# Kernel tuning notes

Measured on AMD Instinct MI355X. Metric: run time of the kernel, lower is better.

The kernel has to match this reference:

```python
import jax, jax.numpy as jnp
import numpy as np

EMBED = 768
HEADS = 12
HEAD = EMBED // HEADS  # 64
NO_ROPE = 1
GRID = 32
S_IMG = GRID * GRID
SEQ = S_IMG + NO_ROPE
BATCH = 8
SCALE = HEAD ** -0.5


def _rope_tables():
    # VisionRotaryEmbeddingFast(dim=half_head_dim=HEAD//2, pt_seq_len=GRID)
    dim = HEAD // 2  # 32 per spatial axis
    inv_freq = 1.0 / (10000.0 ** (np.arange(0, dim, 2, dtype=np.float32) / dim))  # [dim//2]
    t = np.arange(GRID, dtype=np.float32)
    f = t[:, None] * inv_freq[None, :]              # [GRID, dim//2]
    f = np.repeat(f, 2, axis=-1)                    # interleaved pairs -> [GRID, dim]
    fh = np.broadcast_to(f[:, None, :], (GRID, GRID, dim))
    fw = np.broadcast_to(f[None, :, :], (GRID, GRID, dim))
    freqs = np.concatenate([fh, fw], axis=-1).reshape(S_IMG, HEAD)  # [S_IMG, HEAD]
    return jnp.asarray(np.cos(freqs)), jnp.asarray(np.sin(freqs))

ROPE_COS, ROPE_SIN = _rope_tables()


def _rel_pos_index():
    ch, cw = np.meshgrid(np.arange(GRID), np.arange(GRID), indexing='ij')
    coords = np.stack([ch.ravel(), cw.ravel()])          # [2, S_IMG]
    rel = coords[:, :, None] - coords[:, None, :]        # [2, S_IMG, S_IMG]
    rel = rel.transpose(1, 2, 0).astype(np.int64)
    rel[:, :, 0] += GRID - 1
    rel[:, :, 1] += GRID - 1
    rel[:, :, 0] *= 2 * GRID - 1
    return jnp.asarray(rel.sum(-1))                      # [S_IMG, S_IMG]

REL_INDEX = _rel_pos_index()


def _rotate_half(x):
    # pairs are interleaved: (d r) with r=2
    x2 = x.reshape(*x.shape[:-1], -1, 2)
    return jnp.stack([-x2[..., 1], x2[..., 0]], axis=-1).reshape(x.shape)


def _apply_rope(t):
    # t: [B, H, S, HEAD]; first NO_ROPE tokens bypass rope
    t_cls, t_img = t[:, :, :NO_ROPE, :], t[:, :, NO_ROPE:, :]
    t_img = t_img * ROPE_COS + _rotate_half(t_img) * ROPE_SIN
    return jnp.concatenate([t_cls, t_img], axis=2)


def setup_inputs() -> dict:
    key = jax.random.key(0)
    ks = jax.random.split(key, 6)
    std = EMBED ** -0.5
    return {
        'x': jax.random.normal(ks[0], (BATCH, SEQ, EMBED), jnp.float32),
        'qkv_w': jax.random.normal(ks[1], (3 * EMBED, EMBED), jnp.float32) * std,
        'qkv_b': jnp.zeros((3 * EMBED,), jnp.float32),
        'proj_w': jax.random.normal(ks[2], (EMBED, EMBED), jnp.float32) * std,
        'proj_b': jnp.zeros((EMBED,), jnp.float32),
        'rel_bias_table': jax.random.normal(ks[3], ((2 * GRID - 1) * (2 * GRID - 1), HEADS), jnp.float32) * 0.02,
        'key_padding_mask': jnp.zeros((BATCH, SEQ), jnp.bool_),
    }


def reference(x, qkv_w, qkv_b, proj_w, proj_b, rel_bias_table, key_padding_mask):
    B, S, _ = x.shape
    qkv = x @ qkv_w.T + qkv_b                                  # [B,S,3E]
    qkv = qkv.reshape(B, S, 3, HEADS, HEAD).transpose(2, 0, 3, 1, 4)
    q, k, v = qkv[0], qkv[1], qkv[2]                            # [B,H,S,D]
    q = _apply_rope(q)
    k = _apply_rope(k)
    scores = jnp.einsum('bhqd,bhkd->bhqk', q, k) * SCALE        # [B,H,S,S]
    # relative position bias on image-token sub-block
    bias = rel_bias_table[REL_INDEX]                            # [S_IMG,S_IMG,H]
    bias = bias.transpose(2, 0, 1)                              # [H,S_IMG,S_IMG]
    scores = scores.at[:, :, NO_ROPE:, NO_ROPE:].add(bias[None])
    neg = jnp.finfo(scores.dtype).min
    scores = jnp.where(key_padding_mask[:, None, None, :], neg, scores)
    attn = jax.nn.softmax(scores, axis=-1)
    ctx = jnp.einsum('bhqk,bhkd->bhqd', attn, v)
    ctx = ctx.transpose(0, 2, 1, 3).reshape(B, S, EMBED)
    return ctx @ proj_w.T + proj_b
```

## Files before the change

kernel.cpp:

```cpp
#include <hip/hip_runtime.h>
#include <math.h>

#define EMBED 768
#define NHEADS 12
#define HDIM 64
#define SEQ 1025
#define NBATCH 8
#define BHCOUNT (NBATCH*NHEADS)
#define MROWS (NBATCH*SEQ)
#define QKV_N (3*EMBED)
#define QKV_ELEMS (BHCOUNT*SEQ*HDIM)
#define BT_N 3969
#define MASKPAD 1088
#define QMUL 0.1803368801111204f
#define LOG2E 1.4426950408889634f
#define NX4 1574400
#define NW4 442368
#define NP4 147456

typedef __attribute__((ext_vector_type(8))) short bf16x8;
typedef __attribute__((ext_vector_type(4))) float f32x4;
typedef __attribute__((ext_vector_type(16))) float f32x16;
typedef __attribute__((ext_vector_type(4))) unsigned int u32x4;

static __device__ inline unsigned short f2bf(float f) {
    unsigned u = __float_as_uint(f);
    unsigned r = (u + 0x7FFF + ((u >> 16) & 1)) >> 16;
    return (unsigned short)r;
}

static __device__ inline unsigned int cvtpk(float a, float b) {
    unsigned int r;
    asm("v_cvt_pk_bf16_f32 %0, %1, %2" : "=v"(r) : "v"(a), "v"(b));
    return r;
}

static __device__ inline void gld16(const unsigned short* g, unsigned short* l) {
    __builtin_amdgcn_global_load_lds(
        (const __attribute__((address_space(1))) unsigned int*)g,
        (__attribute__((address_space(3))) unsigned int*)l,
        16, 0, 0);
}

__global__ __launch_bounds__(256)
void f2bf3_kernel(const float* __restrict__ x, const float* __restrict__ w,
                  const float* __restrict__ pw,
                  unsigned short* __restrict__ xbf, unsigned short* __restrict__ wbf,
                  unsigned short* __restrict__ pwbf)
{
    int i = blockIdx.x * 256 + threadIdx.x;
    const float* src; unsigned short* dst; int off;
    if (i < NX4)            { src = x;  dst = xbf;  off = i; }
    else if (i < NX4 + NW4) { src = w;  dst = wbf;  off = i - NX4; }
    else if (i < NX4 + NW4 + NP4) { src = pw; dst = pwbf; off = i - NX4 - NW4; }
    else return;
    float4 v = *reinterpret_cast<const float4*>(&src[off << 2]);
    ushort4 o;
    o.x = f2bf(v.x); o.y = f2bf(v.y); o.z = f2bf(v.z); o.w = f2bf(v.w);
    *reinterpret_cast<ushort4*>(&dst[off << 2]) = o;
}

__global__ __launch_bounds__(256)
void setup_tables_kernel(const float* __restrict__ bt, float* __restrict__ btT,
                         const unsigned char* __restrict__ m, unsigned char* __restrict__ mp,
                         float* __restrict__ cosT, float* __restrict__ sinT)
{
    const int bid = blockIdx.x, tid = threadIdx.x;
    if (bid < 256) {
        int s = (bid << 2) + (tid >> 6);
        int d = tid & 63;
        int pos = (d < 32) ? (s >> 5) : (s & 31);
        int j = (d & 31) >> 1;
        float ang = (float)pos * expf(-(float)j * 0.5756462732485115f);
        cosT[(s << 6) + d] = cosf(ang);
        sinT[(s << 6) + d] = sinf(ang);
    } else if (bid < 256 + 187) {
        int e = (bid - 256) * 256 + tid;
        if (e < NHEADS * BT_N) {
            int h = e / BT_N, idx = e - h * BT_N;
            btT[h * BT_N + idx] = bt[idx * NHEADS + h] * LOG2E;
        }
    } else {
        int b = bid - 443;
        for (int i = tid; i < MASKPAD; i += 256)
            mp[b * MASKPAD + i] = (i < SEQ) ? m[b * SEQ + i] : (unsigned char)0;
    }
}

__global__ __launch_bounds__(256)
void qkv_mfma_kernel(const unsigned short* __restrict__ xbf,
                     const unsigned short* __restrict__ wbf,
                     const float* __restrict__ bias,
                     const float* __restrict__ cosT, const float* __restrict__ sinT,
                     unsigned short* __restrict__ qout, unsigned short* __restrict__ kout,
                     unsigned short* __restrict__ vout)
{
    __shared__ unsigned short As[128][32];
    __shared__ unsigned short Bs[128][32];
    const int m0 = blockIdx.x * 128;
    const int n0 = blockIdx.y * 128;
    const int tid = threadIdx.x;
    const int w = tid >> 6, lane = tid & 63;
    const int li = lane & 15, lg = lane >> 4;
    const int wr = w >> 1, wc = w & 1;

    f32x4 acc[4][4];
    #pragma unroll
    for (int mi = 0; mi < 4; ++mi)
        #pragma unroll
        for (int nj = 0; nj < 4; ++nj) acc[mi][nj] = (f32x4){0.f, 0.f, 0.f, 0.f};

    for (int kt = 0; kt < 24; ++kt) {
        const int k0 = kt << 5;
        #pragma unroll
        for (int c = 0; c < 2; ++c) {
            const int idx = c * 256 + tid;
            const int row = idx >> 2, slot = idx & 3;
            int grow = m0 + row; if (grow > MROWS - 1) grow = MROWS - 1;
            gld16(&xbf[(long)grow * EMBED + k0 + slot * 8], &As[0][0] + idx * 8);
            gld16(&wbf[(long)(n0 + row) * EMBED + k0 + slot * 8], &Bs[0][0] + idx * 8);
        }
        __syncthreads();

        bf16x8 af[4], bfr[4];
        #pragma unroll
        for (int mi = 0; mi < 4; ++mi)
            af[mi] = *reinterpret_cast<const bf16x8*>(&As[wr * 64 + mi * 16 + li][lg * 8]);
        #pragma unroll
        for (int nj = 0; nj < 4; ++nj)
            bfr[nj] = *reinterpret_cast<const bf16x8*>(&Bs[wc * 64 + nj * 16 + li][lg * 8]);
        __builtin_amdgcn_s_setprio(1);
        #pragma unroll
        for (int mi = 0; mi < 4; ++mi)
            #pragma unroll
            for (int nj = 0; nj < 4; ++nj)
                acc[mi][nj] = __builtin_amdgcn_mfma_f32_16x16x32_bf16(
                    af[mi], bfr[nj], acc[mi][nj], 0, 0, 0);
        __builtin_amdgcn_s_setprio(0);
        __syncthreads();
    }

    int brow[4][4], srow[4][4];
    #pragma unroll
    for (int mi = 0; mi < 4; ++mi)
        #pragma unroll
        for (int r = 0; r < 4; ++r) {
            int m = m0 + wr * 64 + mi * 16 + lg * 4 + r;
            int mm = (m < MROWS) ? m : (MROWS - 1);
            int bb = mm / SEQ;
            brow[mi][r] = bb;
            srow[mi][r] = mm - bb * SEQ;
        }

    #pragma unroll
    for (int nj = 0; nj < 4; ++nj) {
        const int n = n0 + wc * 64 + nj * 16 + li;
        const int which = n / EMBED;
        const int nh = n - which * EMBED;
        const int h = nh >> 6, d = nh & 63;
        unsigned short* outp = (which == 0) ? qout : (which == 1) ? kout : vout;
        const float mul = (which == 0) ? QMUL : 1.0f;
        const float bn = bias[n];
        const bool dorope = which < 2;
        const float sgn = (d & 1) ? 1.f : -1.f;
        #pragma unroll
        for (int mi = 0; mi < 4; ++mi)
            #pragma unroll
            for (int r = 0; r < 4; ++r) {
                const int m = m0 + wr * 64 + mi * 16 + lg * 4 + r;
                float v = acc[mi][nj][r] + bn;
                float pv = __shfl_xor(v, 1, 64);
                if (m < MROWS) {
                    const int bb = brow[mi][r], s = srow[mi][r];
                    if (dorope && s >= 1) {
                        const int p = s - 1;
                        v = v * cosT[(p << 6) + d] + sgn * pv * sinT[(p << 6) + d];
                    }
                    outp[((long)(bb * NHEADS + h) * SEQ + s) * HDIM + d] = f2bf(v * mul);
                }
            }
    }
}

__global__ __launch_bounds__(256)
void attn_mfma_kernel(const unsigned short* __restrict__ qg,
                      const unsigned short* __restrict__ kg,
                      const unsigned short* __restrict__ vg,
                      const float* __restrict__ btT,
                      const unsigned char* __restrict__ maskpad,
                      unsigned short* __restrict__ ctx)
{
    __shared__ unsigned short Ks[2][64][64];
    __shared__ unsigned short Vts[2][64][64];

    const int i = (int)blockIdx.x;
    const int xcd = i & 7, jb = i >> 3;
    const int bh = xcd * 12 + (jb % 12);
    const int q0 = (jb / 12) * 128;
    const int b = bh / NHEADS, h = bh % NHEADS;
    const int tid = threadIdx.x;
    const int w = tid >> 6;
    const int lane = tid & 63;
    const int l31 = lane & 31;
    const int hi = lane >> 5;

    const unsigned short* qbase = qg + (long)bh * (SEQ * HDIM);
    const unsigned short* kbase = kg + (long)bh * (SEQ * HDIM);
    const unsigned short* vbase = vg + (long)bh * (SEQ * HDIM);
    const unsigned char* maskp = maskpad + b * MASKPAD;
    const float* btTh = btT + h * BT_N;

    const int sidx0 = tid, sidx1 = 256 + tid;
    const int sr0 = sidx0 >> 3, sc0 = (sidx0 & 7) << 3;
    const int sr1 = sidx1 >> 3, sc1 = (sidx1 & 7) << 3;
    const int kswz0 = ((sr0 ^ (sr0 >> 3)) & 7) << 3;
    const int kswz1 = ((sr1 ^ (sr1 >> 3)) & 7) << 3;

    gld16(&kbase[(long)sr0 * HDIM + (sc0 ^ kswz0)], &Ks[0][0][0] + sidx0 * 8);
    gld16(&kbase[(long)sr1 * HDIM + (sc1 ^ kswz1)], &Ks[0][0][0] + sidx1 * 8);
    int4 vreg[2];
    vreg[0] = *reinterpret_cast<const int4*>(&vbase[(long)sr0 * HDIM + sc0]);
    vreg[1] = *reinterpret_cast<const int4*>(&vbase[(long)sr1 * HDIM + sc1]);

    const int qrow = (w << 5) + l31;
    const int qi_l = q0 + qrow;
    const int qiq = (qi_l > SEQ - 1) ? (SEQ - 1) : qi_l;
    bf16x8 qf[4];
    #pragma unroll
    for (int s = 0; s < 4; ++s)
        qf[s] = *reinterpret_cast<const bf16x8*>(&qbase[(long)qiq * HDIM + s * 16 + hi * 8]);

    const float bq = (qi_l >= 1) ? 1.0f : 0.0f;
    int qp = qi_l - 1; if (qp < 0) qp = 0; if (qp > 1023) qp = 1023;
    const int qcode = (qp >> 5) * 63 + (qp & 31) + 1984;

    __syncthreads();
    {
        union { int4 v; unsigned short u[8]; } t0, t1;
        t0.v = vreg[0]; t1.v = vreg[1];
        const int cb30 = sc0 >> 3, cb31 = sc1 >> 3;
        #pragma unroll
        for (int e = 0; e < 8; ++e) {
            Vts[0][sc0 + e][sr0 ^ (((e ^ cb30) & 7) << 3)] = t0.u[e];
            Vts[0][sc1 + e][sr1 ^ (((e ^ cb31) & 7) << 3)] = t1.u[e];
        }
    }
    __syncthreads();

    float m_l = -1e30f, l_l = 0.f;
    f32x16 acco[2];
    #pragma unroll
    for (int r = 0; r < 16; ++r) { acco[0][r] = 0.f; acco[1][r] = 0.f; }

    int kcb[2][4];
    for (int kt = 0; kt < 17; ++kt) {
        const int k0 = kt * 64;
        const int cur = kt & 1;

        if (kt < 16) {
            const int k0n = k0 + 64;
            vreg[0] = (k0n + sr0 < SEQ)
                ? *reinterpret_cast<const int4*>(&vbase[(long)(k0n + sr0) * HDIM + sc0])
                : make_int4(0, 0, 0, 0);
            vreg[1] = (k0n + sr1 < SEQ)
                ? *reinterpret_cast<const int4*>(&vbase[(long)(k0n + sr1) * HDIM + sc1])
                : make_int4(0, 0, 0, 0);
            int ki0 = k0n + sr0; if (ki0 > SEQ - 1) ki0 = SEQ - 1;
            int ki1 = k0n + sr1; if (ki1 > SEQ - 1) ki1 = SEQ - 1;
            gld16(&kbase[(long)ki0 * HDIM + (sc0 ^ kswz0)], &Ks[cur ^ 1][0][0] + sidx0 * 8);
            gld16(&kbase[(long)ki1 * HDIM + (sc1 ^ kswz1)], &Ks[cur ^ 1][0][0] + sidx1 * 8);
        }

        unsigned int b4[2][4];
        float bvf[2][16];
        if (kt >= 1 && kt <= 15) {
            #pragma unroll
            for (int j = 0; j < 2; ++j)
                #pragma unroll
                for (int t = 0; t < 4; ++t) {
                    b4[j][t] = *reinterpret_cast<const unsigned int*>(
                        &maskp[k0 + j * 32 + t * 8 + hi * 4]);
                    kcb[j][t] += 126;
                    const int base = qcode - kcb[j][t];
                    if (t == 0 && hi == 0) {
                        float4 f = *reinterpret_cast<const float4*>(&btTh[base - 34]);
                        bvf[j][0] = btTh[base]; bvf[j][1] = f.z;
                        bvf[j][2] = f.y;        bvf[j][3] = f.x;
                    } else {
                        float4 f = *reinterpret_cast<const float4*>(&btTh[base - 3]);
                        bvf[j][t * 4 + 0] = f.w; bvf[j][t * 4 + 1] = f.z;
                        bvf[j][t * 4 + 2] = f.y; bvf[j][t * 4 + 3] = f.x;
                    }
                }
        } else {
            #pragma unroll
            for (int j = 0; j < 2; ++j)
                #pragma unroll
                for (int t = 0; t < 4; ++t) {
                    unsigned int bb = 0;
                    #pragma unroll
                    for (int ri = 0; ri < 4; ++ri) {
                        const int ki = k0 + j * 32 + t * 8 + hi * 4 + ri;
                        const int kic = (ki > SEQ - 1) ? (SEQ - 1) : ki;
                        unsigned int dead = (ki >= SEQ) ? 1u : (unsigned int)maskp[kic];
                        bb |= (dead ? 1u : 0u) << (ri * 8);
                        int kp = ki - 1; if (kp < 0) kp = 0; if (kp > 1023) kp = 1023;
                        const int kcv = (kp >> 5) * 63 + (kp & 31);
                        bvf[j][t * 4 + ri] = btTh[qcode - kcv];
                    }
                    b4[j][t] = bb;
                    if (kt == 0) {
                        const int kp0 = j * 32 + t * 8 + hi * 4 - 1;
                        kcb[j][t] = (kp0 >> 5) * 63 + (kp0 & 31);
                    }
                }
        }

        f32x16 accs[2];
        #pragma unroll
        for (int r = 0; r < 16; ++r) { accs[0][r] = 0.f; accs[1][r] = 0.f; }
        __builtin_amdgcn_s_setprio(1);
        #pragma unroll
        for (int j = 0; j < 2; ++j) {
            const int rswz = ((l31 ^ (j * 4 + (l31 >> 3))) & 7) << 3;
            const unsigned short* krow = &Ks[cur][j * 32 + l31][0];
            #pragma unroll
            for (int s = 0; s < 4; ++s) {
                bf16x8 kf = *reinterpret_cast<const bf16x8*>(&krow[(s * 16 + hi * 8) ^ rswz]);
                accs[j] = __builtin_amdgcn_mfma_f32_32x32x16_bf16(kf, qf[s], accs[j], 0, 0, 0);
            }
        }
        __builtin_amdgcn_s_setprio(0);

        const float bq00 = (kt == 0 && hi == 0) ? 0.0f : bq;
        accs[0][0] += bvf[0][0] * bq00;
        #pragma unroll
        for (int j = 0; j < 2; ++j)
            #pragma unroll
            for (int r = 0; r < 16; ++r)
                if (!(j == 0 && r == 0))
                    accs[j][r] += bvf[j][r] * bq;
        if (__any((b4[0][0] | b4[0][1] | b4[0][2] | b4[0][3] |
                   b4[1][0] | b4[1][1] | b4[1][2] | b4[1][3]) != 0)) {
            #pragma unroll
            for (int j = 0; j < 2; ++j)
                #pragma unroll
                for (int r = 0; r < 16; ++r)
                    if ((b4[j][r >> 2] >> ((r & 3) * 8)) & 0xFF) accs[j][r] = -1e30f;
        }

        float mx = accs[0][0];
        #pragma unroll
        for (int j = 0; j < 2; ++j)
            #pragma unroll
            for (int r = 0; r < 16; ++r) mx = fmaxf(mx, accs[j][r]);
        mx = fmaxf(mx, __shfl_xor(mx, 32, 64));
        if (__any(mx > m_l + 8.0f)) {
            const float mnew = fmaxf(m_l, mx);
            const float alpha = __builtin_amdgcn_exp2f(m_l - mnew);
            #pragma unroll
            for (int r = 0; r < 16; ++r) {
                const float al = __shfl(alpha, (r & 3) + 8 * (r >> 2) + 4 * hi, 64);
                acco[0][r] *= al;
                acco[1][r] *= al;
            }
            l_l *= alpha;
            m_l = mnew;
        }
        float rs = 0.f;
        #pragma unroll
        for (int j = 0; j < 2; ++j)
            #pragma unroll
            for (int r = 0; r < 16; ++r) {
                accs[j][r] = __builtin_amdgcn_exp2f(accs[j][r] - m_l);
                rs += accs[j][r];
            }
        rs += __shfl_xor(rs, 32, 64);
        l_l += rs;

        unsigned int W[2][8];
        #pragma unroll
        for (int j = 0; j < 2; ++j)
            #pragma unroll
            for (int p = 0; p < 8; ++p)
                W[j][p] = cvtpk(accs[j][2 * p], accs[j][2 * p + 1]);
        #pragma unroll
        for (int j = 0; j < 2; ++j)
            #pragma unroll
            for (int sg = 0; sg < 2; ++sg) {
                unsigned int a0 = W[j][4 * sg + 0], a2 = W[j][4 * sg + 2];
                asm volatile("v_permlane32_swap_b32 %0, %1" : "+v"(a0), "+v"(a2));
                W[j][4 * sg + 0] = a0; W[j][4 * sg + 2] = a2;
                unsigned int a1 = W[j][4 * sg + 1], a3 = W[j][4 * sg + 3];
                asm volatile("v_permlane32_swap_b32 %0, %1" : "+v"(a1), "+v"(a3));
                W[j][4 * sg + 1] = a1; W[j][4 * sg + 3] = a3;
            }

        __builtin_amdgcn_s_setprio(1);
        #pragma unroll
        for (int j2 = 0; j2 < 2; ++j2) {
            const int vswz = ((l31 ^ (j2 * 4 + (l31 >> 3))) & 7) << 3;
            const unsigned short* vrow = &Vts[cur][j2 * 32 + l31][0];
            #pragma unroll
            for (int s = 0; s < 4; ++s) {
                bf16x8 vf = *reinterpret_cast<const bf16x8*>(&vrow[(s * 16 + hi * 8) ^ vswz]);
                u32x4 aw;
                aw[0] = W[s >> 1][4 * (s & 1) + 0];
                aw[1] = W[s >> 1][4 * (s & 1) + 1];
                aw[2] = W[s >> 1][4 * (s & 1) + 2];
                aw[3] = W[s >> 1][4 * (s & 1) + 3];
                bf16x8 pa = __builtin_bit_cast(bf16x8, aw);
                acco[j2] = __builtin_amdgcn_mfma_f32_32x32x16_bf16(pa, vf, acco[j2], 0, 0, 0);
            }
        }
        __builtin_amdgcn_s_setprio(0);

        if (kt < 16) {
            union { int4 v; unsigned short u[8]; } t0, t1;
            t0.v = vreg[0]; t1.v = vreg[1];
            const int cb30 = sc0 >> 3, cb31 = sc1 >> 3;
            #pragma unroll
            for (int e = 0; e < 8; ++e) {
                Vts[cur ^ 1][sc0 + e][sr0 ^ (((e ^ cb30) & 7) << 3)] = t0.u[e];
                Vts[cur ^ 1][sc1 + e][sr1 ^ (((e ^ cb31) & 7) << 3)] = t1.u[e];
            }
            __syncthreads();
        }
    }

    #pragma unroll
    for (int r = 0; r < 16; ++r) {
        const int ql = (r & 3) + 8 * (r >> 2) + 4 * hi;
        const float lb = __shfl(l_l, ql, 64);
        const int qi = q0 + (w << 5) + ql;
        if (qi < SEQ) {
            const float inv = 1.0f / lb;
            ctx[(long)(b * SEQ + qi) * EMBED + h * HDIM + l31] = f2bf(acco[0][r] * inv);
            ctx[(long)(b * SEQ + qi) * EMBED + h * HDIM + 32 + l31] = f2bf(acco[1][r] * inv);
        }
    }
}

__global__ __launch_bounds__(256)
void proj_mfma_kernel(const unsigned short* __restrict__ ctxbf,
                      const unsigned short* __restrict__ pwbf,
                      const float* __restrict__ bias, float* __restrict__ out)
{
    __shared__ unsigned short As[128][32];
    __shared__ unsigned short Bs[128][32];
    const int m0 = blockIdx.x * 128;
    const int n0 = blockIdx.y * 128;
    const int tid = threadIdx.x;
    const int w = tid >> 6, lane = tid & 63;
    const int li = lane & 15, lg = lane >> 4;
    const int wr = w >> 1, wc = w & 1;

    f32x4 acc[4][4];
    #pragma unroll
    for (int mi = 0; mi < 4; ++mi)
        #pragma unroll
        for (int nj = 0; nj < 4; ++nj) acc[mi][nj] = (f32x4){0.f, 0.f, 0.f, 0.f};

    for (int kt = 0; kt < 24; ++kt) {
        const int k0 = kt << 5;
        #pragma unroll
        for (int c = 0; c < 2; ++c) {
            const int idx = c * 256 + tid;
            const int row = idx >> 2, slot = idx & 3;
            int grow = m0 + row; if (grow > MROWS - 1) grow = MROWS - 1;
            gld16(&ctxbf[(long)grow * EMBED + k0 + slot * 8], &As[0][0] + idx * 8);
            gld16(&pwbf[(long)(n0 + row) * EMBED + k0 + slot * 8], &Bs[0][0] + idx * 8);
        }
        __syncthreads();

        bf16x8 af[4], bfr[4];
        #pragma unroll
        for (int mi = 0; mi < 4; ++mi)
            af[mi] = *reinterpret_cast<const bf16x8*>(&As[wr * 64 + mi * 16 + li][lg * 8]);
        #pragma unroll
        for (int nj = 0; nj < 4; ++nj)
            bfr[nj] = *reinterpret_cast<const bf16x8*>(&Bs[wc * 64 + nj * 16 + li][lg * 8]);
        __builtin_amdgcn_s_setprio(1);
        #pragma unroll
        for (int mi = 0; mi < 4; ++mi)
            #pragma unroll
            for (int nj = 0; nj < 4; ++nj)
                acc[mi][nj] = __builtin_amdgcn_mfma_f32_16x16x32_bf16(
                    af[mi], bfr[nj], acc[mi][nj], 0, 0, 0);
        __builtin_amdgcn_s_setprio(0);
        __syncthreads();
    }

    #pragma unroll
    for (int nj = 0; nj < 4; ++nj) {
        const int n = n0 + wc * 64 + nj * 16 + li;
        const float bn = bias[n];
        #pragma unroll
        for (int mi = 0; mi < 4; ++mi)
            #pragma unroll
            for (int r = 0; r < 4; ++r) {
                const int m = m0 + wr * 64 + mi * 16 + lg * 4 + r;
                if (m < MROWS)
                    out[(long)m * EMBED + n] = acc[mi][nj][r] + bn;
            }
    }
}

extern "C" void kernel_launch(void* const* d_in, const int* in_sizes, int n_in,
                              void* d_out, int out_size, void* d_ws, size_t ws_size,
                              hipStream_t stream) {
    const float* x       = (const float*)d_in[0];
    const float* qkv_w   = (const float*)d_in[1];
    const float* qkv_b   = (const float*)d_in[2];
    const float* proj_w  = (const float*)d_in[3];
    const float* proj_b  = (const float*)d_in[4];
    const float* rel_bt  = (const float*)d_in[5];
    const unsigned char* kmask = (const unsigned char*)d_in[6];
    float* out = (float*)d_out;

    unsigned short* qbuf  = (unsigned short*)d_ws;
    unsigned short* kbuf  = qbuf + QKV_ELEMS;
    unsigned short* vbuf  = kbuf + QKV_ELEMS;
    unsigned short* ctxbf = vbuf + QKV_ELEMS;
    unsigned short* xbf   = ctxbf + QKV_ELEMS;
    unsigned short* wbf   = xbf + QKV_ELEMS;
    unsigned short* pwbf  = wbf + QKV_N * EMBED;
    float* cosT = (float*)(pwbf + EMBED * EMBED);
    float* sinT = cosT + 1024 * HDIM;
    float* btT  = sinT + 1024 * HDIM;
    unsigned char* maskpad = (unsigned char*)(btT + NHEADS * BT_N);

    const int ntot4 = NX4 + NW4 + NP4;
    f2bf3_kernel<<<(ntot4 + 255) / 256, 256, 0, stream>>>(x, qkv_w, proj_w, xbf, wbf, pwbf);
    setup_tables_kernel<<<256 + 187 + NBATCH, 256, 0, stream>>>(
        rel_bt, btT, kmask, maskpad, cosT, sinT);

    qkv_mfma_kernel<<<dim3((MROWS + 127) / 128, QKV_N / 128), 256, 0, stream>>>(
        xbf, wbf, qkv_b, cosT, sinT, qbuf, kbuf, vbuf);
    attn_mfma_kernel<<<9 * BHCOUNT, 256, 0, stream>>>(
        qbuf, kbuf, vbuf, btT, maskpad, ctxbf);
    proj_mfma_kernel<<<dim3((MROWS + 127) / 128, EMBED / 128), 256, 0, stream>>>(
        ctxbf, pwbf, proj_b, out);
}
```

Baseline: 225.1 us.

## Split attention over key range into two halves with a merge kernel

Splits each query tile's key loop into two halves (9 and 8 key tiles), doubling the attention grid from 864 to 1728 blocks so more of the GPU's compute units are busy. Each half writes unnormalized fp32 partial outputs plus running max and sum to a workspace. A new merge kernel combines the two halves with log-sum-exp weighting and writes the bf16 context. The cost is an extra kernel launch and fp32 partial traffic of roughly 50MB written and then read back.

```diff
diff --git a/kernel.cpp b/kernel.cpp
--- a/kernel.cpp
+++ b/kernel.cpp
@@ -12,6 +12,7 @@
 #define QKV_ELEMS (BHCOUNT*SEQ*HDIM)
 #define BT_N 3969
 #define MASKPAD 1088
+#define QPAD 1152
 #define QMUL 0.1803368801111204f
 #define LOG2E 1.4426950408889634f
 #define NX4 1574400
@@ -188,7 +189,7 @@
                       const unsigned short* __restrict__ vg,
                       const float* __restrict__ btT,
                       const unsigned char* __restrict__ maskpad,
-                      unsigned short* __restrict__ ctx)
+                      float* __restrict__ partO, float* __restrict__ partML)
 {
     __shared__ unsigned short Ks[2][64][64];
     __shared__ unsigned short Vts[2][64][64];
@@ -196,7 +197,11 @@
     const int i = (int)blockIdx.x;
     const int xcd = i & 7, jb = i >> 3;
     const int bh = xcd * 12 + (jb % 12);
-    const int q0 = (jb / 12) * 128;
+    const int rest = jb / 12;
+    const int qt = rest % 9;
+    const int sp = rest / 9;
+    const int q0 = qt * 128;
+    const int ktb = sp ? 9 : 0, kte = sp ? 17 : 9;
     const int b = bh / NHEADS, h = bh % NHEADS;
     const int tid = threadIdx.x;
     const int w = tid >> 6;
@@ -216,11 +221,19 @@
     const int kswz0 = ((sr0 ^ (sr0 >> 3)) & 7) << 3;
     const int kswz1 = ((sr1 ^ (sr1 >> 3)) & 7) << 3;
 
-    gld16(&kbase[(long)sr0 * HDIM + (sc0 ^ kswz0)], &Ks[0][0][0] + sidx0 * 8);
-    gld16(&kbase[(long)sr1 * HDIM + (sc1 ^ kswz1)], &Ks[0][0][0] + sidx1 * 8);
+    {
+        int ki0 = ktb * 64 + sr0; if (ki0 > SEQ - 1) ki0 = SEQ - 1;
+        int ki1 = ktb * 64 + sr1; if (ki1 > SEQ - 1) ki1 = SEQ - 1;
+        gld16(&kbase[(long)ki0 * HDIM + (sc0 ^ kswz0)], &Ks[0][0][0] + sidx0 * 8);
+        gld16(&kbase[(long)ki1 * HDIM + (sc1 ^ kswz1)], &Ks[0][0][0] + sidx1 * 8);
+    }
     int4 vreg[2];
-    vreg[0] = *reinterpret_cast<const int4*>(&vbase[(long)sr0 * HDIM + sc0]);
-    vreg[1] = *reinterpret_cast<const int4*>(&vbase[(long)sr1 * HDIM + sc1]);
+    vreg[0] = (ktb * 64 + sr0 < SEQ)
+        ? *reinterpret_cast<const int4*>(&vbase[(long)(ktb * 64 + sr0) * HDIM + sc0])
+        : make_int4(0, 0, 0, 0);
+    vreg[1] = (ktb * 64 + sr1 < SEQ)
+        ? *reinterpret_cast<const int4*>(&vbase[(long)(ktb * 64 + sr1) * HDIM + sc1])
+        : make_int4(0, 0, 0, 0);
 
     const int qrow = (w << 5) + l31;
     const int qi_l = q0 + qrow;
@@ -253,11 +266,11 @@
     for (int r = 0; r < 16; ++r) { acco[0][r] = 0.f; acco[1][r] = 0.f; }
 
     int kcb[2][4];
-    for (int kt = 0; kt < 17; ++kt) {
+    for (int kt = ktb; kt < kte; ++kt) {
         const int k0 = kt * 64;
-        const int cur = kt & 1;
-
-        if (kt < 16) {
+        const int cur = (kt - ktb) & 1;
+
+        if (kt + 1 < kte) {
             const int k0n = k0 + 64;
             vreg[0] = (k0n + sr0 < SEQ)
                 ? *reinterpret_cast<const int4*>(&vbase[(long)(k0n + sr0) * HDIM + sc0])
@@ -273,7 +286,7 @@
 
         unsigned int b4[2][4];
         float bvf[2][16];
-        if (kt >= 1 && kt <= 15) {
+        if (kt > ktb && kt < 16) {
             #pragma unroll
             for (int j = 0; j < 2; ++j)
                 #pragma unroll
@@ -309,8 +322,8 @@
                         bvf[j][t * 4 + ri] = btTh[qcode - kcv];
                     }
                     b4[j][t] = bb;
-                    if (kt == 0) {
-                        const int kp0 = j * 32 + t * 8 + hi * 4 - 1;
+                    if (kt == ktb) {
+                        const int kp0 = k0 + j * 32 + t * 8 + hi * 4 - 1;
                         kcb[j][t] = (kp0 >> 5) * 63 + (kp0 & 31);
                     }
                 }
@@ -415,7 +428,7 @@
         }
         __builtin_amdgcn_s_setprio(0);
 
-        if (kt < 16) {
+        if (kt + 1 < kte) {
             union { int4 v; unsigned short u[8]; } t0, t1;
             t0.v = vreg[0]; t1.v = vreg[1];
             const int cb30 = sc0 >> 3, cb31 = sc1 >> 3;
@@ -428,17 +441,51 @@
         }
     }
 
+    const long pbase = (long)(sp * BHCOUNT + bh) * QPAD * 64;
     #pragma unroll
     for (int r = 0; r < 16; ++r) {
         const int ql = (r & 3) + 8 * (r >> 2) + 4 * hi;
-        const float lb = __shfl(l_l, ql, 64);
-        const int qi = q0 + (w << 5) + ql;
-        if (qi < SEQ) {
-            const float inv = 1.0f / lb;
-            ctx[(long)(b * SEQ + qi) * EMBED + h * HDIM + l31] = f2bf(acco[0][r] * inv);
-            ctx[(long)(b * SEQ + qi) * EMBED + h * HDIM + 32 + l31] = f2bf(acco[1][r] * inv);
-        }
-    }
+        const int prow = q0 + (w << 5) + ql;
+        partO[pbase + (long)prow * 64 + l31]      = acco[0][r];
+        partO[pbase + (long)prow * 64 + 32 + l31] = acco[1][r];
+    }
+    if (hi == 0) {
+        const int prow = q0 + (w << 5) + l31;
+        float* mlp = partML + ((long)(sp * BHCOUNT + bh) * QPAD + prow) * 2;
+        mlp[0] = m_l; mlp[1] = l_l;
+    }
+}
+
+__global__ __launch_bounds__(256)
+void attn_merge_kernel(const float* __restrict__ partO, const float* __restrict__ partML,
+                       unsigned short* __restrict__ ctx)
+{
+    const long idx = (long)blockIdx.x * 256 + threadIdx.x;
+    if (idx >= (long)BHCOUNT * SEQ * 32) return;
+    const int dpair = (int)(idx & 31);
+    const long t = idx >> 5;
+    const int qi = (int)(t % SEQ);
+    const int bh = (int)(t / SEQ);
+    const int b = bh / NHEADS, h = bh - b * NHEADS;
+
+    const float2 ml1 = *reinterpret_cast<const float2*>(
+        &partML[((long)bh * QPAD + qi) * 2]);
+    const float2 ml2 = *reinterpret_cast<const float2*>(
+        &partML[((long)(BHCOUNT + bh) * QPAD + qi) * 2]);
+    const float M = fmaxf(ml1.x, ml2.x);
+    const float w1 = __builtin_amdgcn_exp2f(ml1.x - M);
+    const float w2 = __builtin_amdgcn_exp2f(ml2.x - M);
+    const float inv = 1.0f / (w1 * ml1.y + w2 * ml2.y);
+
+    const int d = dpair << 1;
+    const float2 o1 = *reinterpret_cast<const float2*>(
+        &partO[((long)bh * QPAD + qi) * 64 + d]);
+    const float2 o2 = *reinterpret_cast<const float2*>(
+        &partO[((long)(BHCOUNT + bh) * QPAD + qi) * 64 + d]);
+    const float v0 = (w1 * o1.x + w2 * o2.x) * inv;
+    const float v1 = (w1 * o1.y + w2 * o2.y) * inv;
+    *reinterpret_cast<unsigned int*>(
+        &ctx[((long)(b * SEQ + qi)) * EMBED + h * HDIM + d]) = cvtpk(v0, v1);
 }
 
 __global__ __launch_bounds__(256)
@@ -529,6 +576,8 @@
     float* sinT = cosT + 1024 * HDIM;
     float* btT  = sinT + 1024 * HDIM;
     unsigned char* maskpad = (unsigned char*)(btT + NHEADS * BT_N);
+    float* partO  = (float*)(maskpad + NBATCH * MASKPAD);
+    float* partML = partO + (long)2 * BHCOUNT * QPAD * 64;
 
     const int ntot4 = NX4 + NW4 + NP4;
     f2bf3_kernel<<<(ntot4 + 255) / 256, 256, 0, stream>>>(x, qkv_w, proj_w, xbf, wbf, pwbf);
@@ -537,8 +586,11 @@
 
     qkv_mfma_kernel<<<dim3((MROWS + 127) / 128, QKV_N / 128), 256, 0, stream>>>(
         xbf, wbf, qkv_b, cosT, sinT, qbuf, kbuf, vbuf);
-    attn_mfma_kernel<<<9 * BHCOUNT, 256, 0, stream>>>(
-        qbuf, kbuf, vbuf, btT, maskpad, ctxbf);
+    attn_mfma_kernel<<<2 * 9 * BHCOUNT, 256, 0, stream>>>(
+        qbuf, kbuf, vbuf, btT, maskpad, partO, partML);
+    const long nmerge = (long)BHCOUNT * SEQ * 32;
+    attn_merge_kernel<<<(int)((nmerge + 255) / 256), 256, 0, stream>>>(
+        partO, partML, ctxbf);
     proj_mfma_kernel<<<dim3((MROWS + 127) / 128, EMBED / 128), 256, 0, stream>>>(
         ctxbf, pwbf, proj_b, out);
 }
```

Result: slower. 245.8 us (+9.2%).
